# Optimization experiments

Measured on AMD Instinct MI355X. Metric: run time of the kernel, lower is better.

## Reference

```python
import jax, jax.numpy as jnp
import numpy as np

N, E, D, H, C, G, L = 50000, 1250000, 128, 64, 10, 128, 2


def setup_inputs() -> dict:
    key = jax.random.key(0)
    ks = jax.random.split(key, 18)
    s = lambda fan_in: 1.0 / np.sqrt(fan_in)
    inp = {
        "x": jax.random.normal(ks[0], (N, D), dtype=jnp.float32),
        "edge_index": jax.random.randint(ks[1], (2, E), 0, N, dtype=jnp.int64),
        "batch": jnp.sort(jax.random.randint(ks[2], (N,), 0, G, dtype=jnp.int64)),
        # node embedding MLP (D->H->H)
        "emb_w1": jax.random.uniform(ks[3], (D, H), jnp.float32, -s(D), s(D)),
        "emb_b1": jnp.zeros((H,), jnp.float32),
        "emb_w2": jax.random.uniform(ks[4], (H, H), jnp.float32, -s(H), s(H)),
        "emb_b2": jnp.zeros((H,), jnp.float32),
        # per-conv-block params, stacked over L layers
        "rel_w": jax.random.uniform(ks[5], (L, H, H), jnp.float32, -s(H), s(H)),
        "rel_b": jnp.zeros((L, H), jnp.float32),
        "root_w": jax.random.uniform(ks[6], (L, H, H), jnp.float32, -s(H), s(H)),
        "post_w1": jax.random.uniform(ks[7], (L, H, H), jnp.float32, -s(H), s(H)),
        "post_b1": jnp.zeros((L, H), jnp.float32),
        "post_w2": jax.random.uniform(ks[8], (L, H, H), jnp.float32, -s(H), s(H)),
        "post_b2": jnp.zeros((L, H), jnp.float32),
        # classifier
        "cls_w": jax.random.uniform(ks[9], (H, C), jnp.float32, -s(H), s(H)),
        "cls_b": jnp.zeros((C,), jnp.float32),
    }
    return inp


def _mlp(h, w1, b1, w2, b2):
    # Linear -> relu -> (dropout: identity in eval) -> Linear
    return jax.nn.relu(h @ w1 + b1) @ w2 + b2


def reference(x, edge_index, batch, emb_w1, emb_b1, emb_w2, emb_b2,
              rel_w, rel_b, root_w, post_w1, post_b1, post_w2, post_b2,
              cls_w, cls_b):
    src, dst = edge_index[0], edge_index[1]
    h = _mlp(x, emb_w1, emb_b1, emb_w2, emb_b2)  # [N,H]
    deg = jax.ops.segment_sum(jnp.ones((E,), h.dtype), dst, num_segments=N)
    inv_deg = 1.0 / jnp.maximum(deg, 1.0)  # mean aggregation, isolated nodes -> 0
    for l in range(L):
        agg = jax.ops.segment_sum(h[src], dst, num_segments=N) * inv_deg[:, None]
        h = agg @ rel_w[l] + rel_b[l] + h @ root_w[l]  # GraphConv (lin_root bias-free)
        h = _mlp(h, post_w1[l], post_b1[l], post_w2[l], post_b2[l])
        h = jax.nn.relu(h)  # dropout is identity in eval
    cnt = jax.ops.segment_sum(jnp.ones((N,), h.dtype), batch, num_segments=G)
    pooled = jax.ops.segment_sum(h, batch, num_segments=G) / jnp.maximum(cnt, 1.0)[:, None]
    return pooled @ cls_w + cls_b  # [G,C]
```

## Files before the change

### kernel.cpp

```cpp
#include <hip/hip_runtime.h>

typedef unsigned int u32;
typedef unsigned short u16;

#define NN 50000
#define EE 1250000
#define DD 128
#define HH 64
#define NCLS 10
#define NG 128
#define MAXDEG 80

#define NTILES ((NN + 63) / 64)
#define LDSW 68

#define PBUK 392
#define SBLK 128
#define CHUNK ((EE + SBLK - 1) / SBLK)
#define NDP  (PBUK * 128)


__device__ __forceinline__ u32 f2bf(float f) {
    u32 u = __float_as_uint(f);
    return (u + 0x7FFFu + ((u >> 16) & 1u)) >> 16;
}
__device__ __forceinline__ float bf2f(u16 v) {
    return __uint_as_float(((u32)v) << 16);
}


__device__ __forceinline__ void load_w(const float* __restrict__ g, float (*wS)[LDSW], int t) {
    #pragma unroll
    for (int r = 0; r < 4; ++r) {
        int idx = r * 256 + t;
        int k = idx >> 4, f4 = idx & 15;
        float4 v = *(const float4*)(g + k * 64 + f4 * 4);
        *(float4*)&wS[k][f4 * 4] = v;
    }
}

__device__ __forceinline__ void load_inT(const float* __restrict__ g, int ld, int c0,
                                         float (*iS)[LDSW], int t, int nb) {
    #pragma unroll
    for (int r = 0; r < 4; ++r) {
        int idx = r * 256 + t;
        int n = idx >> 4, k4 = idx & 15;
        int node = nb + n;
        if (node >= NN) node = NN - 1;
        float4 v = *(const float4*)(g + (size_t)node * ld + c0 + k4 * 4);
        int k0 = k4 * 4;
        int nx = n ^ k0;
        iS[k0 + 0][nx] = v.x;
        iS[k0 + 1][nx] = v.y;
        iS[k0 + 2][nx] = v.z;
        iS[k0 + 3][nx] = v.w;
    }
}

__device__ __forceinline__ void load_inT_hb(const u16* __restrict__ g,
                                            float (*iS)[LDSW], int t, int nb) {
    #pragma unroll
    for (int r = 0; r < 2; ++r) {
        int idx = r * 256 + t;
        int n = idx >> 3, c = idx & 7;
        int node = nb + n;
        if (node >= NN) node = NN - 1;
        uint4 v = *(const uint4*)(g + (size_t)node * HH + c * 8);
        int k0 = c * 8;
        int nx1 = n ^ k0;
        int nx2 = n ^ (k0 + 4);
        iS[k0 + 0][nx1] = bf2f((u16)(v.x & 0xffffu));
        iS[k0 + 1][nx1] = bf2f((u16)(v.x >> 16));
        iS[k0 + 2][nx1] = bf2f((u16)(v.y & 0xffffu));
        iS[k0 + 3][nx1] = bf2f((u16)(v.y >> 16));
        iS[k0 + 4][nx2] = bf2f((u16)(v.z & 0xffffu));
        iS[k0 + 5][nx2] = bf2f((u16)(v.z >> 16));
        iS[k0 + 6][nx2] = bf2f((u16)(v.w & 0xffffu));
        iS[k0 + 7][nx2] = bf2f((u16)(v.w >> 16));
    }
}

__device__ __forceinline__ void gemm_acc(const float (*iS)[LDSW], const float (*wS)[LDSW],
                                         float acc[4][4], int tx, int ty) {
    #pragma unroll 8
    for (int k = 0; k < 64; ++k) {
        const float4 wv = *(const float4*)&wS[k][tx * 4];
        const float4 iv = *(const float4*)&iS[k][(ty * 4) ^ (k & 60)];
        acc[0][0] += iv.x * wv.x; acc[0][1] += iv.x * wv.y; acc[0][2] += iv.x * wv.z; acc[0][3] += iv.x * wv.w;
        acc[1][0] += iv.y * wv.x; acc[1][1] += iv.y * wv.y; acc[1][2] += iv.y * wv.z; acc[1][3] += iv.y * wv.w;
        acc[2][0] += iv.z * wv.x; acc[2][1] += iv.z * wv.y; acc[2][2] += iv.z * wv.z; acc[2][3] += iv.z * wv.w;
        acc[3][0] += iv.w * wv.x; acc[3][1] += iv.w * wv.y; acc[3][2] += iv.w * wv.z; acc[3][3] += iv.w * wv.w;
    }
}

__device__ __forceinline__ void store_accT(float (*iS)[LDSW], const float acc[4][4], int tx, int ty) {
    #pragma unroll
    for (int i = 0; i < 4; ++i) {
        int k = tx * 4 + i;
        *(float4*)&iS[k][(ty * 4) ^ (tx * 4)] =
            make_float4(acc[0][i], acc[1][i], acc[2][i], acc[3][i]);
    }
}

__device__ __forceinline__ void init_bias(float acc[4][4], const float* __restrict__ b, int tx) {
    float4 bv = *(const float4*)(b + tx * 4);
    #pragma unroll
    for (int j = 0; j < 4; ++j) { acc[j][0] = bv.x; acc[j][1] = bv.y; acc[j][2] = bv.z; acc[j][3] = bv.w; }
}

__device__ __forceinline__ void relu_acc(float acc[4][4]) {
    #pragma unroll
    for (int j = 0; j < 4; ++j)
        #pragma unroll
        for (int i = 0; i < 4; ++i) acc[j][i] = fmaxf(acc[j][i], 0.0f);
}

__device__ __forceinline__ void store_hb(u16* __restrict__ hb, const float acc[4][4],
                                         int tx, int ty, int nb) {
    #pragma unroll
    for (int j = 0; j < 4; ++j) {
        int node = nb + ty * 4 + j;
        if (node < NN) {
            u32 p0 = f2bf(acc[j][0]) | (f2bf(acc[j][1]) << 16);
            u32 p1 = f2bf(acc[j][2]) | (f2bf(acc[j][3]) << 16);
            u32* q = (u32*)(hb + (size_t)node * HH) + tx * 2;
            q[0] = p0; q[1] = p1;
        }
    }
}


__global__ __launch_bounds__(256) void k_embed_psort(
    const float* __restrict__ x,
    const float* __restrict__ w1, const float* __restrict__ b1,
    const float* __restrict__ w2, const float* __restrict__ b2,
    u16* __restrict__ hb,
    const int* __restrict__ ei, u32* __restrict__ bedges,
    int* __restrict__ gboff, int* __restrict__ ghist) {
    __shared__ __align__(16) char smem[2 * 64 * LDSW * 4];
    const int t = threadIdx.x;

    if (blockIdx.x < NTILES) {
        float (*wS)[LDSW] = (float (*)[LDSW])smem;
        float (*iS)[LDSW] = (float (*)[LDSW])(smem + 64 * LDSW * 4);
        const int tx = t & 15, ty = t >> 4;
        const int nb = blockIdx.x * 64;

        float acc[4][4];
        init_bias(acc, b1, tx);
        load_w(w1, wS, t);
        load_inT(x, DD, 0, iS, t, nb);
        __syncthreads();
        gemm_acc(iS, wS, acc, tx, ty);
        __syncthreads();
        load_w(w1 + 64 * 64, wS, t);
        load_inT(x, DD, 64, iS, t, nb);
        __syncthreads();
        gemm_acc(iS, wS, acc, tx, ty);
        __syncthreads();
        relu_acc(acc);
        store_accT(iS, acc, tx, ty);
        load_w(w2, wS, t);
        __syncthreads();
        float acc2[4][4];
        init_bias(acc2, b2, tx);
        gemm_acc(iS, wS, acc2, tx, ty);
        store_hb(hb, acc2, tx, ty, nb);
    } else {
        int* hist  = (int*)smem;
        int* boffS = hist + PBUK;
        int* wsum  = boffS + PBUK;
        const int cb = blockIdx.x - NTILES;
        const int base = cb * CHUNK;
        const int n = min(CHUNK, EE - base);

        for (int b = t; b < PBUK; b += 256) hist[b] = 0;
        __syncthreads();
        for (int i = t; i < n; i += 256) {
            int src = ei[base + i];
            int dst = ei[EE + base + i];
            if ((unsigned)src < NN && (unsigned)dst < NN)
                atomicAdd(&hist[dst >> 7], 1);
        }
        __syncthreads();
        int v = 0, h0 = 0;
        if (t < PBUK / 2) { h0 = hist[2 * t]; v = h0 + hist[2 * t + 1]; }
        int lane = t & 63, wd = t >> 6;
        int incl = v;
        #pragma unroll
        for (int d = 1; d < 64; d <<= 1) {
            int tt = __shfl_up(incl, d);
            if (lane >= d) incl += tt;
        }
        if (lane == 63) wsum[wd] = incl;
        __syncthreads();
        int woff = 0;
        for (int w = 0; w < wd; ++w) woff += wsum[w];
        if (t < PBUK / 2) {
            int excl = woff + incl - v;
            boffS[2 * t] = excl;
            boffS[2 * t + 1] = excl + h0;
        }
        __syncthreads();
        for (int b = t; b < PBUK; b += 256) {
            gboff[cb * PBUK + b] = boffS[b];
            ghist[cb * PBUK + b] = hist[b];
        }
        __syncthreads();
        for (int b = t; b < PBUK; b += 256) hist[b] = 0;
        __syncthreads();
        for (int i = t; i < n; i += 256) {
            int src = ei[base + i];
            int dst = ei[EE + base + i];
            if ((unsigned)src < NN && (unsigned)dst < NN) {
                int b = dst >> 7;
                int p = atomicAdd(&hist[b], 1);
                bedges[base + boffS[b] + p] = ((u32)src << 7) | (u32)(dst & 127);
            }
        }
    }
}


__global__ __launch_bounds__(256) void k_adj(const u32* __restrict__ bedges,
                                             const int* __restrict__ gboff,
                                             const int* __restrict__ ghist,
                                             u16* __restrict__ slots,
                                             int* __restrict__ deg,
                                             float* __restrict__ pooled) {
    __shared__ u16 ls[128 * MAXDEG];
    __shared__ int lc[128];
    const int b = blockIdx.x, t = threadIdx.x;
    const int lane = t & 63, wid = t >> 6;
    if (b < (NG * HH) / 256) pooled[b * 256 + t] = 0.0f;
    if (t < 128) lc[t] = 0;
    __syncthreads();
    for (int sb = wid; sb < SBLK; sb += 4) {
        int off = gboff[sb * PBUK + b];
        int cnt = ghist[sb * PBUK + b];
        int gbase = sb * CHUNK + off;
        for (int i = lane; i < cnt; i += 64) {
            u32 p = bedges[gbase + i];
            int o = (int)(p & 127u);
            int src = (int)(p >> 7);
            int pos = atomicAdd(&lc[o], 1);
            if (pos < MAXDEG) ls[o * MAXDEG + pos] = (u16)src;
        }
    }
    __syncthreads();
    u32* gs = (u32*)(slots + (size_t)b * 128 * MAXDEG);
    const u32* lsu = (const u32*)ls;
    for (int i = t; i < 128 * MAXDEG / 2; i += 256) gs[i] = lsu[i];
    if (t < 128) deg[b * 128 + t] = lc[t];
}


__global__ __launch_bounds__(256) void k_agg(
    const u16* __restrict__ hb, const int* __restrict__ deg,
    const u16* __restrict__ slots, float* __restrict__ agg) {
    const int wid = threadIdx.x >> 6, lane = threadIdx.x & 63;
    const int nA = blockIdx.x * 8 + wid * 2;
    if (nA >= NN) return;
    const int nB = nA + 1;
    const int dA = deg[nA];
    const int dB = (nB < NN) ? deg[nB] : 0;
    const int mA = min(dA, MAXDEG), mB = min(dB, MAXDEG);
    const u16* srA = slots + (size_t)nA * MAXDEG;
    const u16* srB = slots + (size_t)nB * MAXDEG;
    const u32* rowA = (const u32*)srA;
    const u32* rowB = (const u32*)srB;
    float sA = 0.0f, sB = 0.0f;
    const int mm = max(mA, mB);
    for (int e = 0; e + 8 <= mm; e += 8) {
        const int hx = e >> 1;
        const bool pA = (e + 8 <= mA), pB = (e + 8 <= mB);
        float a0=0,a1=0,a2=0,a3=0,a4=0,a5=0,a6=0,a7=0;
        float b0=0,b1=0,b2=0,b3=0,b4=0,b5=0,b6=0,b7=0;
        if (pA) {
            u32 u0 = rowA[hx], u1 = rowA[hx+1], u2 = rowA[hx+2], u3 = rowA[hx+3];
            a0 = bf2f(hb[(size_t)(u0 & 0xffffu) * HH + lane]);
            a1 = bf2f(hb[(size_t)(u0 >> 16) * HH + lane]);
            a2 = bf2f(hb[(size_t)(u1 & 0xffffu) * HH + lane]);
            a3 = bf2f(hb[(size_t)(u1 >> 16) * HH + lane]);
            a4 = bf2f(hb[(size_t)(u2 & 0xffffu) * HH + lane]);
            a5 = bf2f(hb[(size_t)(u2 >> 16) * HH + lane]);
            a6 = bf2f(hb[(size_t)(u3 & 0xffffu) * HH + lane]);
            a7 = bf2f(hb[(size_t)(u3 >> 16) * HH + lane]);
        }
        if (pB) {
            u32 u0 = rowB[hx], u1 = rowB[hx+1], u2 = rowB[hx+2], u3 = rowB[hx+3];
            b0 = bf2f(hb[(size_t)(u0 & 0xffffu) * HH + lane]);
            b1 = bf2f(hb[(size_t)(u0 >> 16) * HH + lane]);
            b2 = bf2f(hb[(size_t)(u1 & 0xffffu) * HH + lane]);
            b3 = bf2f(hb[(size_t)(u1 >> 16) * HH + lane]);
            b4 = bf2f(hb[(size_t)(u2 & 0xffffu) * HH + lane]);
            b5 = bf2f(hb[(size_t)(u2 >> 16) * HH + lane]);
            b6 = bf2f(hb[(size_t)(u3 & 0xffffu) * HH + lane]);
            b7 = bf2f(hb[(size_t)(u3 >> 16) * HH + lane]);
        }
        if (pA) sA += ((a0 + a1) + (a2 + a3)) + ((a4 + a5) + (a6 + a7));
        if (pB) sB += ((b0 + b1) + (b2 + b3)) + ((b4 + b5) + (b6 + b7));
    }
    for (int e = mA & ~7; e < mA; ++e)
        sA += bf2f(hb[(size_t)srA[e] * HH + lane]);
    for (int e = mB & ~7; e < mB; ++e)
        sB += bf2f(hb[(size_t)srB[e] * HH + lane]);
    agg[(size_t)nA * HH + lane] = sA * (1.0f / (float)max(dA, 1));
    if (nB < NN)
        agg[(size_t)nB * HH + lane] = sB * (1.0f / (float)max(dB, 1));
}


__global__ __launch_bounds__(256) void k_dense(
    u16* hb, const float* __restrict__ agg,
    const float* __restrict__ relw, const float* __restrict__ relb,
    const float* __restrict__ rootw,
    const float* __restrict__ pw1, const float* __restrict__ pb1,
    const float* __restrict__ pw2, const float* __restrict__ pb2,
    const int* __restrict__ batch, float* __restrict__ pooled, int do_pool) {
    __shared__ float wS[64][LDSW];
    __shared__ float iS[64][LDSW];
    const int t = threadIdx.x;
    const int tx = t & 15, ty = t >> 4;
    const int nb = blockIdx.x * 64;

    float acc[4][4];
    init_bias(acc, relb, tx);

    load_w(relw, wS, t);
    load_inT(agg, HH, 0, iS, t, nb);
    __syncthreads();
    gemm_acc(iS, wS, acc, tx, ty);
    __syncthreads();
    load_w(rootw, wS, t);
    load_inT_hb(hb, iS, t, nb);
    __syncthreads();
    gemm_acc(iS, wS, acc, tx, ty);
    __syncthreads();
    store_accT(iS, acc, tx, ty);
    load_w(pw1, wS, t);
    __syncthreads();
    float acc2[4][4];
    init_bias(acc2, pb1, tx);
    gemm_acc(iS, wS, acc2, tx, ty);
    relu_acc(acc2);
    __syncthreads();
    store_accT(iS, acc2, tx, ty);
    load_w(pw2, wS, t);
    __syncthreads();
    float acc3[4][4];
    init_bias(acc3, pb2, tx);
    gemm_acc(iS, wS, acc3, tx, ty);
    relu_acc(acc3);

    if (!do_pool) {
        store_hb(hb, acc3, tx, ty, nb);
    } else {
        __syncthreads();
        store_accT(iS, acc3, tx, ty);
        __syncthreads();
        if (t < HH) {
            const int f = t;
            const int fs = f & 60;
            const int n1 = min(64, NN - nb);
            int cur = batch[nb];
            float s = 0.0f;
            for (int i = 0; i < n1; ++i) {
                int g = batch[nb + i];
                if (g != cur) {
                    if ((unsigned)cur < NG) atomicAdd(&pooled[cur * HH + f], s);
                    s = 0.0f; cur = g;
                }
                s += iS[f][i ^ fs];
            }
            if ((unsigned)cur < NG) atomicAdd(&pooled[cur * HH + f], s);
        }
    }
}


__global__ void k_cls(const float* __restrict__ pooled, const int* __restrict__ batch,
                      const float* __restrict__ w, const float* __restrict__ b,
                      float* __restrict__ out) {
    const int g = blockIdx.x;
    const int t = threadIdx.x;
    if (t >= NCLS) return;
    int lo = 0, hi = NN;
    while (lo < hi) { int mid = (lo + hi) >> 1; if (batch[mid] < g) lo = mid + 1; else hi = mid; }
    const int beg = lo;
    lo = 0; hi = NN;
    while (lo < hi) { int mid = (lo + hi) >> 1; if (batch[mid] < g + 1) lo = mid + 1; else hi = mid; }
    const int cnt = lo - beg;
    const float inv = 1.0f / (float)max(cnt, 1);
    float o = b[t];
    #pragma unroll 8
    for (int k = 0; k < HH; ++k) o += pooled[g * HH + k] * inv * w[k * NCLS + t];
    out[g * NCLS + t] = o;
}


extern "C" void kernel_launch(void* const* d_in, const int* in_sizes, int n_in,
                              void* d_out, int out_size, void* d_ws, size_t ws_size,
                              hipStream_t stream) {
    const float* x      = (const float*)d_in[0];
    const int*   ei     = (const int*)d_in[1];
    const int*   batch  = (const int*)d_in[2];
    const float* emb_w1 = (const float*)d_in[3];
    const float* emb_b1 = (const float*)d_in[4];
    const float* emb_w2 = (const float*)d_in[5];
    const float* emb_b2 = (const float*)d_in[6];
    const float* rel_w  = (const float*)d_in[7];
    const float* rel_b  = (const float*)d_in[8];
    const float* root_w = (const float*)d_in[9];
    const float* pw1    = (const float*)d_in[10];
    const float* pb1    = (const float*)d_in[11];
    const float* pw2    = (const float*)d_in[12];
    const float* pb2    = (const float*)d_in[13];
    const float* cls_w  = (const float*)d_in[14];
    const float* cls_b  = (const float*)d_in[15];
    float* out = (float*)d_out;

    char* ws = (char*)d_ws;
    size_t off = 0;
    auto alloc = [&](size_t bytes) -> void* {
        off = (off + 255) & ~(size_t)255;
        void* p = ws + off;
        off += bytes;
        return p;
    };
    u16*   hb     = (u16*)alloc((size_t)NN * HH * 2);
    float* agg    = (float*)alloc((size_t)NN * HH * 4);
    u32*   bedges = (u32*)agg;
    u16*   slots  = (u16*)alloc((size_t)NDP * MAXDEG * 2);
    int*   deg    = (int*)alloc((size_t)NDP * 4);
    int*   gboff  = (int*)alloc((size_t)SBLK * PBUK * 4);
    int*   ghist  = (int*)alloc((size_t)SBLK * PBUK * 4);
    float* pooled = (float*)alloc((size_t)NG * HH * 4);

    k_embed_psort<<<NTILES + SBLK, 256, 0, stream>>>(
        x, emb_w1, emb_b1, emb_w2, emb_b2, hb, ei, bedges, gboff, ghist);
    k_adj<<<PBUK, 256, 0, stream>>>(bedges, gboff, ghist, slots, deg, pooled);
    k_agg<<<(NN + 7) / 8, 256, 0, stream>>>(hb, deg, slots, agg);
    k_dense<<<NTILES, 256, 0, stream>>>(hb, agg, rel_w, rel_b, root_w,
                                        pw1, pb1, pw2, pb2, batch, pooled, 0);
    k_agg<<<(NN + 7) / 8, 256, 0, stream>>>(hb, deg, slots, agg);
    k_dense<<<NTILES, 256, 0, stream>>>(hb, agg,
                                        rel_w + HH * HH, rel_b + HH, root_w + HH * HH,
                                        pw1 + HH * HH, pb1 + HH, pw2 + HH * HH, pb2 + HH,
                                        batch, pooled, 1);
    k_cls<<<NG, 64, 0, stream>>>(pooled, batch, cls_w, cls_b, out);
}
```

Before: 308.7 us.

## Use bf16 MFMA with hi/lo split weights in dense GraphConv layers

Rewrites the per-layer dense kernel to use 16x16x32 bf16 MFMA instructions instead of scalar fp32 FMA tiles. The layer weights are pre-transposed and split into bf16 hi and lo parts by extra blocks in the embed/partition kernel. The aggregation output is also stored as bf16, which halves agg traffic. Intermediate activations are rounded to bf16 between GEMMs, trading some accuracy for fewer LDS passes and higher matrix throughput.

```diff
diff --git a/kernel.cpp b/kernel.cpp
--- a/kernel.cpp
+++ b/kernel.cpp
@@ -19,6 +19,9 @@
 #define CHUNK ((EE + SBLK - 1) / SBLK)
 #define NDP  (PBUK * 128)
 
+#define NWMAT 8
+#define WT_LO (NWMAT * 4096)
+
 
 __device__ __forceinline__ u32 f2bf(float f) {
     u32 u = __float_as_uint(f);
@@ -27,6 +30,9 @@
 __device__ __forceinline__ float bf2f(u16 v) {
     return __uint_as_float(((u32)v) << 16);
 }
+
+typedef __attribute__((ext_vector_type(8))) short bf16x8;
+typedef __attribute__((ext_vector_type(4))) float f32x4;
 
 
 __device__ __forceinline__ void load_w(const float* __restrict__ g, float (*wS)[LDSW], int t) {
@@ -57,29 +63,6 @@
     }
 }
 
-__device__ __forceinline__ void load_inT_hb(const u16* __restrict__ g,
-                                            float (*iS)[LDSW], int t, int nb) {
-    #pragma unroll
-    for (int r = 0; r < 2; ++r) {
-        int idx = r * 256 + t;
-        int n = idx >> 3, c = idx & 7;
-        int node = nb + n;
-        if (node >= NN) node = NN - 1;
-        uint4 v = *(const uint4*)(g + (size_t)node * HH + c * 8);
-        int k0 = c * 8;
-        int nx1 = n ^ k0;
-        int nx2 = n ^ (k0 + 4);
-        iS[k0 + 0][nx1] = bf2f((u16)(v.x & 0xffffu));
-        iS[k0 + 1][nx1] = bf2f((u16)(v.x >> 16));
-        iS[k0 + 2][nx1] = bf2f((u16)(v.y & 0xffffu));
-        iS[k0 + 3][nx1] = bf2f((u16)(v.y >> 16));
-        iS[k0 + 4][nx2] = bf2f((u16)(v.z & 0xffffu));
-        iS[k0 + 5][nx2] = bf2f((u16)(v.z >> 16));
-        iS[k0 + 6][nx2] = bf2f((u16)(v.w & 0xffffu));
-        iS[k0 + 7][nx2] = bf2f((u16)(v.w >> 16));
-    }
-}
-
 __device__ __forceinline__ void gemm_acc(const float (*iS)[LDSW], const float (*wS)[LDSW],
                                          float acc[4][4], int tx, int ty) {
     #pragma unroll 8
@@ -136,7 +119,10 @@
     const float* __restrict__ w2, const float* __restrict__ b2,
     u16* __restrict__ hb,
     const int* __restrict__ ei, u32* __restrict__ bedges,
-    int* __restrict__ gboff, int* __restrict__ ghist) {
+    int* __restrict__ gboff, int* __restrict__ ghist,
+    const float* __restrict__ rel_w, const float* __restrict__ root_w,
+    const float* __restrict__ pw1, const float* __restrict__ pw2,
+    u16* __restrict__ wtb) {
     __shared__ __align__(16) char smem[2 * 64 * LDSW * 4];
     const int t = threadIdx.x;
 
@@ -166,7 +152,7 @@
         init_bias(acc2, b2, tx);
         gemm_acc(iS, wS, acc2, tx, ty);
         store_hb(hb, acc2, tx, ty, nb);
-    } else {
+    } else if (blockIdx.x < NTILES + SBLK) {
         int* hist  = (int*)smem;
         int* boffS = hist + PBUK;
         int* wsum  = boffS + PBUK;
@@ -217,6 +203,30 @@
                 int p = atomicAdd(&hist[b], 1);
                 bedges[base + boffS[b] + p] = ((u32)src << 7) | (u32)(dst & 127);
             }
+        }
+    } else {
+        const int m = blockIdx.x - NTILES - SBLK;
+        const int layer = m >> 2, which = m & 3;
+        const float* srcw =
+            (which == 0 ? rel_w : which == 1 ? root_w : which == 2 ? pw1 : pw2)
+            + (size_t)layer * HH * HH;
+        float* ldsf = (float*)smem;
+        #pragma unroll
+        for (int r = 0; r < 16; ++r) {
+            int idx = r * 256 + t;
+            int k = idx >> 6, n = idx & 63;
+            ldsf[k * 65 + n] = srcw[k * 64 + n];
+        }
+        __syncthreads();
+        #pragma unroll
+        for (int r = 0; r < 16; ++r) {
+            int idx = r * 256 + t;
+            int n = idx >> 6, k = idx & 63;
+            float v = ldsf[k * 65 + n];
+            u16 hi = (u16)f2bf(v);
+            u16 lo = (u16)f2bf(v - bf2f(hi));
+            wtb[m * 4096 + n * 64 + k] = hi;
+            wtb[WT_LO + m * 4096 + n * 64 + k] = lo;
         }
     }
 }
@@ -257,7 +267,7 @@
 
 __global__ __launch_bounds__(256) void k_agg(
     const u16* __restrict__ hb, const int* __restrict__ deg,
-    const u16* __restrict__ slots, float* __restrict__ agg) {
+    const u16* __restrict__ slots, u16* __restrict__ aggb) {
     const int wid = threadIdx.x >> 6, lane = threadIdx.x & 63;
     const int nA = blockIdx.x * 8 + wid * 2;
     if (nA >= NN) return;
@@ -305,63 +315,124 @@
         sA += bf2f(hb[(size_t)srA[e] * HH + lane]);
     for (int e = mB & ~7; e < mB; ++e)
         sB += bf2f(hb[(size_t)srB[e] * HH + lane]);
-    agg[(size_t)nA * HH + lane] = sA * (1.0f / (float)max(dA, 1));
+    aggb[(size_t)nA * HH + lane] = (u16)f2bf(sA * (1.0f / (float)max(dA, 1)));
     if (nB < NN)
-        agg[(size_t)nB * HH + lane] = sB * (1.0f / (float)max(dB, 1));
+        aggb[(size_t)nB * HH + lane] = (u16)f2bf(sB * (1.0f / (float)max(dB, 1)));
 }
 
 
 __global__ __launch_bounds__(256) void k_dense(
-    u16* hb, const float* __restrict__ agg,
-    const float* __restrict__ relw, const float* __restrict__ relb,
-    const float* __restrict__ rootw,
-    const float* __restrict__ pw1, const float* __restrict__ pb1,
-    const float* __restrict__ pw2, const float* __restrict__ pb2,
+    u16* __restrict__ hb, const u16* __restrict__ aggb,
+    const u16* __restrict__ wt,
+    const float* __restrict__ relb,
+    const float* __restrict__ pb1, const float* __restrict__ pb2,
     const int* __restrict__ batch, float* __restrict__ pooled, int do_pool) {
-    __shared__ float wS[64][LDSW];
-    __shared__ float iS[64][LDSW];
+    __shared__ __align__(16) u16 acts[2][64][72];
     const int t = threadIdx.x;
-    const int tx = t & 15, ty = t >> 4;
+    const int w = t >> 6;
+    const int l = t & 63;
+    const int lr = l & 15, lg = l >> 4;
+    const int rowb = w * 16;
     const int nb = blockIdx.x * 64;
-
-    float acc[4][4];
-    init_bias(acc, relb, tx);
-
-    load_w(relw, wS, t);
-    load_inT(agg, HH, 0, iS, t, nb);
+    int nodeA = nb + rowb + lr;
+    if (nodeA >= NN) nodeA = NN - 1;
+
+    const u16* w_rel = wt;
+    const u16* w_root = wt + 4096;
+    const u16* w_p1  = wt + 2 * 4096;
+    const u16* w_p2  = wt + 3 * 4096;
+
+    const u16* agp = aggb + (size_t)nodeA * HH + lg * 8;
+    const u16* hbp = hb   + (size_t)nodeA * HH + lg * 8;
+    bf16x8 a0 = *(const bf16x8*)agp;
+    bf16x8 a1 = *(const bf16x8*)(agp + 32);
+    bf16x8 h0 = *(const bf16x8*)hbp;
+    bf16x8 h1 = *(const bf16x8*)(hbp + 32);
+
+    f32x4 acc[4];
+    #pragma unroll
+    for (int tt = 0; tt < 4; ++tt) {
+        float b = relb[tt * 16 + lr];
+        acc[tt] = (f32x4){b, b, b, b};
+    }
+    #pragma unroll
+    for (int tt = 0; tt < 4; ++tt) {
+        const u16* pr = w_rel  + (tt * 16 + lr) * 64 + lg * 8;
+        const u16* po = w_root + (tt * 16 + lr) * 64 + lg * 8;
+        acc[tt] = __builtin_amdgcn_mfma_f32_16x16x32_bf16(a0, *(const bf16x8*)pr,                acc[tt], 0, 0, 0);
+        acc[tt] = __builtin_amdgcn_mfma_f32_16x16x32_bf16(a1, *(const bf16x8*)(pr + 32),         acc[tt], 0, 0, 0);
+        acc[tt] = __builtin_amdgcn_mfma_f32_16x16x32_bf16(a0, *(const bf16x8*)(pr + WT_LO),      acc[tt], 0, 0, 0);
+        acc[tt] = __builtin_amdgcn_mfma_f32_16x16x32_bf16(a1, *(const bf16x8*)(pr + WT_LO + 32), acc[tt], 0, 0, 0);
+        acc[tt] = __builtin_amdgcn_mfma_f32_16x16x32_bf16(h0, *(const bf16x8*)po,                acc[tt], 0, 0, 0);
+        acc[tt] = __builtin_amdgcn_mfma_f32_16x16x32_bf16(h1, *(const bf16x8*)(po + 32),         acc[tt], 0, 0, 0);
+        acc[tt] = __builtin_amdgcn_mfma_f32_16x16x32_bf16(h0, *(const bf16x8*)(po + WT_LO),      acc[tt], 0, 0, 0);
+        acc[tt] = __builtin_amdgcn_mfma_f32_16x16x32_bf16(h1, *(const bf16x8*)(po + WT_LO + 32), acc[tt], 0, 0, 0);
+    }
+    #pragma unroll
+    for (int tt = 0; tt < 4; ++tt)
+        #pragma unroll
+        for (int r = 0; r < 4; ++r)
+            acts[0][rowb + lg * 4 + r][tt * 16 + lr] = (u16)f2bf(acc[tt][r]);
     __syncthreads();
-    gemm_acc(iS, wS, acc, tx, ty);
+
+    bf16x8 c0 = *(const bf16x8*)&acts[0][rowb + lr][lg * 8];
+    bf16x8 c1 = *(const bf16x8*)&acts[0][rowb + lr][32 + lg * 8];
+    f32x4 acc2[4];
+    #pragma unroll
+    for (int tt = 0; tt < 4; ++tt) {
+        float b = pb1[tt * 16 + lr];
+        acc2[tt] = (f32x4){b, b, b, b};
+    }
+    #pragma unroll
+    for (int tt = 0; tt < 4; ++tt) {
+        const u16* pr = w_p1 + (tt * 16 + lr) * 64 + lg * 8;
+        acc2[tt] = __builtin_amdgcn_mfma_f32_16x16x32_bf16(c0, *(const bf16x8*)pr,                acc2[tt], 0, 0, 0);
+        acc2[tt] = __builtin_amdgcn_mfma_f32_16x16x32_bf16(c1, *(const bf16x8*)(pr + 32),         acc2[tt], 0, 0, 0);
+        acc2[tt] = __builtin_amdgcn_mfma_f32_16x16x32_bf16(c0, *(const bf16x8*)(pr + WT_LO),      acc2[tt], 0, 0, 0);
+        acc2[tt] = __builtin_amdgcn_mfma_f32_16x16x32_bf16(c1, *(const bf16x8*)(pr + WT_LO + 32), acc2[tt], 0, 0, 0);
+    }
+    #pragma unroll
+    for (int tt = 0; tt < 4; ++tt)
+        #pragma unroll
+        for (int r = 0; r < 4; ++r)
+            acts[1][rowb + lg * 4 + r][tt * 16 + lr] = (u16)f2bf(fmaxf(acc2[tt][r], 0.0f));
     __syncthreads();
-    load_w(rootw, wS, t);
-    load_inT_hb(hb, iS, t, nb);
-    __syncthreads();
-    gemm_acc(iS, wS, acc, tx, ty);
-    __syncthreads();
-    store_accT(iS, acc, tx, ty);
-    load_w(pw1, wS, t);
-    __syncthreads();
-    float acc2[4][4];
-    init_bias(acc2, pb1, tx);
-    gemm_acc(iS, wS, acc2, tx, ty);
-    relu_acc(acc2);
-    __syncthreads();
-    store_accT(iS, acc2, tx, ty);
-    load_w(pw2, wS, t);
-    __syncthreads();
-    float acc3[4][4];
-    init_bias(acc3, pb2, tx);
-    gemm_acc(iS, wS, acc3, tx, ty);
-    relu_acc(acc3);
+
+    bf16x8 d0 = *(const bf16x8*)&acts[1][rowb + lr][lg * 8];
+    bf16x8 d1 = *(const bf16x8*)&acts[1][rowb + lr][32 + lg * 8];
+    f32x4 acc3[4];
+    #pragma unroll
+    for (int tt = 0; tt < 4; ++tt) {
+        float b = pb2[tt * 16 + lr];
+        acc3[tt] = (f32x4){b, b, b, b};
+    }
+    #pragma unroll
+    for (int tt = 0; tt < 4; ++tt) {
+        const u16* pr = w_p2 + (tt * 16 + lr) * 64 + lg * 8;
+        acc3[tt] = __builtin_amdgcn_mfma_f32_16x16x32_bf16(d0, *(const bf16x8*)pr,                acc3[tt], 0, 0, 0);
+        acc3[tt] = __builtin_amdgcn_mfma_f32_16x16x32_bf16(d1, *(const bf16x8*)(pr + 32),         acc3[tt], 0, 0, 0);
+        acc3[tt] = __builtin_amdgcn_mfma_f32_16x16x32_bf16(d0, *(const bf16x8*)(pr + WT_LO),      acc3[tt], 0, 0, 0);
+        acc3[tt] = __builtin_amdgcn_mfma_f32_16x16x32_bf16(d1, *(const bf16x8*)(pr + WT_LO + 32), acc3[tt], 0, 0, 0);
+    }
 
     if (!do_pool) {
-        store_hb(hb, acc3, tx, ty, nb);
+        #pragma unroll
+        for (int tt = 0; tt < 4; ++tt)
+            #pragma unroll
+            for (int r = 0; r < 4; ++r) {
+                int node = nb + rowb + lg * 4 + r;
+                if (node < NN)
+                    hb[(size_t)node * HH + tt * 16 + lr] = (u16)f2bf(fmaxf(acc3[tt][r], 0.0f));
+            }
     } else {
-        __syncthreads();
-        store_accT(iS, acc3, tx, ty);
+        #pragma unroll
+        for (int tt = 0; tt < 4; ++tt)
+            #pragma unroll
+            for (int r = 0; r < 4; ++r)
+                acts[0][rowb + lg * 4 + r][tt * 16 + lr] = (u16)f2bf(fmaxf(acc3[tt][r], 0.0f));
         __syncthreads();
         if (t < HH) {
             const int f = t;
-            const int fs = f & 60;
             const int n1 = min(64, NN - nb);
             int cur = batch[nb];
             float s = 0.0f;
@@ -371,7 +442,7 @@
                     if ((unsigned)cur < NG) atomicAdd(&pooled[cur * HH + f], s);
                     s = 0.0f; cur = g;
                 }
-                s += iS[f][i ^ fs];
+                s += bf2f(acts[0][i][f]);
             }
             if ((unsigned)cur < NG) atomicAdd(&pooled[cur * HH + f], s);
         }
@@ -429,24 +500,24 @@
         return p;
     };
     u16*   hb     = (u16*)alloc((size_t)NN * HH * 2);
-    float* agg    = (float*)alloc((size_t)NN * HH * 4);
-    u32*   bedges = (u32*)agg;
+    u16*   aggb   = (u16*)alloc((size_t)NN * HH * 2);
+    u32*   bedges = (u32*)aggb;
     u16*   slots  = (u16*)alloc((size_t)NDP * MAXDEG * 2);
     int*   deg    = (int*)alloc((size_t)NDP * 4);
     int*   gboff  = (int*)alloc((size_t)SBLK * PBUK * 4);
     int*   ghist  = (int*)alloc((size_t)SBLK * PBUK * 4);
     float* pooled = (float*)alloc((size_t)NG * HH * 4);
-
-    k_embed_psort<<<NTILES + SBLK, 256, 0, stream>>>(
-        x, emb_w1, emb_b1, emb_w2, emb_b2, hb, ei, bedges, gboff, ghist);
+    u16*   wtb    = (u16*)alloc((size_t)2 * NWMAT * 4096 * 2);
+
+    k_embed_psort<<<NTILES + SBLK + NWMAT, 256, 0, stream>>>(
+        x, emb_w1, emb_b1, emb_w2, emb_b2, hb, ei, bedges, gboff, ghist,
+        rel_w, root_w, pw1, pw2, wtb);
     k_adj<<<PBUK, 256, 0, stream>>>(bedges, gboff, ghist, slots, deg, pooled);
-    k_agg<<<(NN + 7) / 8, 256, 0, stream>>>(hb, deg, slots, agg);
-    k_dense<<<NTILES, 256, 0, stream>>>(hb, agg, rel_w, rel_b, root_w,
-                                        pw1, pb1, pw2, pb2, batch, pooled, 0);
-    k_agg<<<(NN + 7) / 8, 256, 0, stream>>>(hb, deg, slots, agg);
-    k_dense<<<NTILES, 256, 0, stream>>>(hb, agg,
-                                        rel_w + HH * HH, rel_b + HH, root_w + HH * HH,
-                                        pw1 + HH * HH, pb1 + HH, pw2 + HH * HH, pb2 + HH,
+    k_agg<<<(NN + 7) / 8, 256, 0, stream>>>(hb, deg, slots, aggb);
+    k_dense<<<NTILES, 256, 0, stream>>>(hb, aggb, wtb, rel_b, pb1, pb2, batch, pooled, 0);
+    k_agg<<<(NN + 7) / 8, 256, 0, stream>>>(hb, deg, slots, aggb);
+    k_dense<<<NTILES, 256, 0, stream>>>(hb, aggb, wtb + 4 * 4096,
+                                        rel_b + HH, pb1 + HH, pb2 + HH,
                                         batch, pooled, 1);
     k_cls<<<NG, 64, 0, stream>>>(pooled, batch, cls_w, cls_b, out);
 }
```

Result: slower. 316.0 us (+2.4%).
